# Optimization experiments

Measured on AMD Instinct MI355X. Metric: run time of the kernel, lower is better.

The kernel has to match this reference:

```python
import jax, jax.numpy as jnp
import numpy as np

DIM = 512
HEADS = 8
HEAD_DIM = DIM // HEADS
SCALE = DIM ** (-0.5)  # source uses full dim, not head_dim
LAMBDA_COND = 1.0


def setup_inputs() -> dict:
    key = jax.random.key(0)
    ks = jax.random.split(key, 16)
    b, n, m_a, m_s = 4, 2048, 2048, 256
    s = 0.02
    inp = {
        "x": jax.random.normal(ks[0], (b, n, DIM), jnp.float32),
        "audio_context": jax.random.normal(ks[1], (b, m_a, DIM), jnp.float32),
        "singer_context": jax.random.normal(ks[2], (b, m_s, DIM), jnp.float32),
        "Wq": jax.random.normal(ks[3], (DIM, DIM), jnp.float32) * s,
        "bq": jnp.zeros((DIM,), jnp.float32),
        "Wka": jax.random.normal(ks[4], (DIM, DIM), jnp.float32) * s,
        "bka": jnp.zeros((DIM,), jnp.float32),
        "Wva": jax.random.normal(ks[5], (DIM, DIM), jnp.float32) * s,
        "bva": jnp.zeros((DIM,), jnp.float32),
        "Wks": jax.random.normal(ks[6], (DIM, DIM), jnp.float32) * s,
        "bks": jnp.zeros((DIM,), jnp.float32),
        "Wvs": jax.random.normal(ks[7], (DIM, DIM), jnp.float32) * s,
        "bvs": jnp.zeros((DIM,), jnp.float32),
        "Wp": jax.random.normal(ks[8], (DIM, DIM), jnp.float32) * s,
        "bp": jnp.zeros((DIM,), jnp.float32),
    }
    return inp


def _heads(t):
    b, n, c = t.shape
    return t.reshape(b, n, HEADS, HEAD_DIM).transpose(0, 2, 1, 3)  # (b,h,n,d)


def _attend(q, ctx, Wk, bk, Wv, bv):
    k = _heads(ctx @ Wk.T + bk)
    v = _heads(ctx @ Wv.T + bv)
    attn = jax.nn.softmax(jnp.einsum("bhnd,bhmd->bhnm", q, k) * SCALE, axis=-1)
    o = jnp.einsum("bhnm,bhmd->bhnd", attn, v)
    b, h, n, d = o.shape
    return o.transpose(0, 2, 1, 3).reshape(b, n, h * d)


def reference(x, audio_context, singer_context, Wq, bq, Wka, bka, Wva, bva,
              Wks, bks, Wvs, bvs, Wp, bp):
    q = _heads(x @ Wq.T + bq)
    x_audio = _attend(q, audio_context, Wka, bka, Wva, bva)
    x_singer = _attend(q, singer_context, Wks, bks, Wvs, bvs)
    out = x_audio + LAMBDA_COND * x_singer
    return out @ Wp.T + bp
```

## Files before the change

kernel.cpp:

```cpp
#include <hip/hip_runtime.h>

#define DIM 512
#define NQ 2048
#define MA 2048
#define MS 256
#define QSCALE 0.06375864651f

typedef __attribute__((ext_vector_type(8))) short bf16x8;
typedef __attribute__((ext_vector_type(4))) float f32x4;
typedef __attribute__((ext_vector_type(16))) float f32x16;

__device__ __forceinline__ ushort f2b(float f) {
    uint u = __float_as_uint(f);
    u = (u + 0x7fffu + ((u >> 16) & 1u)) >> 16;
    return (ushort)u;
}

__device__ __forceinline__ uint pk2bf(float a, float b) {
#if __has_builtin(__builtin_amdgcn_cvt_pk_bf16_f32)
    typedef __attribute__((ext_vector_type(2))) __bf16 bf2;
    bf2 r = __builtin_amdgcn_cvt_pk_bf16_f32(a, b);
    uint u;
    __builtin_memcpy(&u, &r, 4);
    return u;
#else
    return ((__float_as_uint(a) + 0x8000u) >> 16) |
           ((__float_as_uint(b) + 0x8000u) & 0xffff0000u);
#endif
}

__device__ __forceinline__ float fexp2(float x) {
#if __has_builtin(__builtin_amdgcn_exp2f)
    return __builtin_amdgcn_exp2f(x);
#else
    return exp2f(x);
#endif
}

__device__ __forceinline__ void gload16(const ushort* g, ushort* l) {
    __builtin_amdgcn_global_load_lds(
        (const __attribute__((address_space(1))) void*)g,
        (__attribute__((address_space(3))) void*)l, 16, 0, 0);
}

__global__ __launch_bounds__(256) void cast_all(const float* __restrict__ w0,
                                                const float* __restrict__ w1,
                                                const float* __restrict__ w2,
                                                const float* __restrict__ w3,
                                                const float* __restrict__ w4,
                                                const float* __restrict__ w5,
                                                const float* __restrict__ x,
                                                const float* __restrict__ ac,
                                                const float* __restrict__ scx,
                                                ushort* __restrict__ dst) {
    int i = blockIdx.x * 256 + threadIdx.x;
    const float* s;
    int o;
    if (i < 393216) {
        int w = i >> 16;
        s = w < 3 ? (w == 0 ? w0 : (w == 1 ? w1 : w2))
                  : (w == 3 ? w3 : (w == 4 ? w4 : w5));
        o = i & 65535;
    } else if (i < 1441792) { s = x;   o = i - 393216; }
    else if (i < 2490368)   { s = ac;  o = i - 1441792; }
    else                    { s = scx; o = i - 2490368; }
    float4 v = ((const float4*)s)[o];
    ushort4 u;
    u.x = f2b(v.x); u.y = f2b(v.y); u.z = f2b(v.z); u.w = f2b(v.w);
    ((ushort4*)dst)[i] = u;
}

struct GD {
    const ushort* A; const ushort* B; const float* bias; void* out;
    long sB, sO;
    int N, bx, by, blk0, biasrow, scaleq, outf32, pad;
};

__global__ __launch_bounds__(256) void gemm_fused(GD d0, GD d1, GD d2, GD d3, GD d4) {
    __shared__ ushort At[128 * 32];
    __shared__ ushort Bt[128 * 32];
    GD d = d0;
    int bid = blockIdx.x;
    if (bid >= d1.blk0) d = d1;
    if (bid >= d2.blk0) d = d2;
    if (bid >= d3.blk0) d = d3;
    if (bid >= d4.blk0) d = d4;
    int local = bid - d.blk0;
    int x = local % d.bx;
    int rem = local / d.bx;
    int y = rem % d.by;
    int z = rem / d.by;

    int t = threadIdx.x;
    int wv = t >> 6, ln = t & 63, l = ln & 15, g = ln >> 4;
    int wrow = wv & 1, wcol = wv >> 1;
    int row0 = x * 128, col0 = y * 128;
    int srow = t >> 2;
    int slot = (t & 3) * 8;
    int sko = ((t ^ srow) & 3) * 8;
    int kc8 = ((g ^ (l & 3)) & 3) * 8;
    const ushort* Ab = d.A;
    const ushort* Bb = d.B + (size_t)z * d.sB;
    int N = d.N;

    f32x4 acc[4][4];
#pragma unroll
    for (int i = 0; i < 4; i++)
#pragma unroll
        for (int j = 0; j < 4; j++) acc[i][j] = (f32x4){0, 0, 0, 0};

    for (int k0 = 0; k0 < 512; k0 += 32) {
        __syncthreads();
#pragma unroll
        for (int c = 0; c < 2; c++) {
            gload16(Ab + (size_t)(row0 + srow + 64 * c) * 512 + k0 + sko,
                    At + (srow + 64 * c) * 32 + slot);
            gload16(Bb + (size_t)(col0 + srow + 64 * c) * 512 + k0 + sko,
                    Bt + (srow + 64 * c) * 32 + slot);
        }
        __syncthreads();
        bf16x8 ar[4], br[4];
#pragma unroll
        for (int i = 0; i < 4; i++)
            ar[i] = *(const bf16x8*)(At + (wrow * 64 + i * 16 + l) * 32 + kc8);
#pragma unroll
        for (int j = 0; j < 4; j++)
            br[j] = *(const bf16x8*)(Bt + (wcol * 64 + j * 16 + l) * 32 + kc8);
#pragma unroll
        for (int i = 0; i < 4; i++)
#pragma unroll
            for (int j = 0; j < 4; j++)
                acc[i][j] = __builtin_amdgcn_mfma_f32_16x16x32_bf16(ar[i], br[j], acc[i][j], 0, 0, 0);
    }
#pragma unroll
    for (int i = 0; i < 4; i++) {
#pragma unroll
        for (int j = 0; j < 4; j++) {
            int row = row0 + wrow * 64 + i * 16 + g * 4;
            int col = col0 + wcol * 64 + j * 16 + l;
#pragma unroll
            for (int r = 0; r < 4; r++) {
                float bv = d.biasrow ? d.bias[row + r] : d.bias[col];
                float o = acc[i][j][r] + bv;
                if (d.scaleq) o *= QSCALE;
                if (d.outf32)
                    ((float*)d.out + (size_t)z * d.sO)[(size_t)(row + r) * N + col] = o;
                else
                    ((ushort*)d.out + (size_t)z * d.sO)[(size_t)(row + r) * N + col] = f2b(o);
            }
        }
    }
}

__device__ __forceinline__ void attn_ctx32(const ushort* __restrict__ kg,
                                           const ushort* __restrict__ vg,
                                           int M, int nt, const bf16x8 (&aq)[4],
                                           ushort* __restrict__ Kl,
                                           ushort* __restrict__ Vl,
                                           f32x16 (&o)[2], float& li,
                                           int l5, int hi, int sr, int sc, int vbase) {
    bf16x8 k0 = *(const bf16x8*)kg;
    bf16x8 k1 = *(const bf16x8*)(kg + (size_t)32 * DIM);
    bf16x8 v0 = *(const bf16x8*)vg;
    bf16x8 v1 = *(const bf16x8*)(vg + (size_t)32 * M);
    __syncthreads();
    {
        *(bf16x8*)(Kl + sr * 72 + sc) = k0;
        *(bf16x8*)(Kl + (sr + 32) * 72 + sc) = k1;
        union { bf16x8 v; uint2 h[2]; } cv;
        cv.v = v0;
        *(uint2*)(Vl + sr * 72 + vbase) = cv.h[0];
        *(uint2*)(Vl + sr * 72 + vbase + 8) = cv.h[1];
        cv.v = v1;
        *(uint2*)(Vl + (sr + 32) * 72 + vbase) = cv.h[0];
        *(uint2*)(Vl + (sr + 32) * 72 + vbase + 8) = cv.h[1];
    }
    if (nt > 1) {
        k0 = *(const bf16x8*)(kg + (size_t)64 * DIM);
        k1 = *(const bf16x8*)(kg + (size_t)96 * DIM);
        v0 = *(const bf16x8*)(vg + 64);
        v1 = *(const bf16x8*)(vg + (size_t)32 * M + 64);
    }
    for (int i = 0; i < nt; i++) {
        __syncthreads();
        if (i + 1 < nt) {
            ushort* Kb = Kl + ((i + 1) & 1) * (64 * 72);
            ushort* Vb = Vl + ((i + 1) & 1) * (64 * 72);
            *(bf16x8*)(Kb + sr * 72 + sc) = k0;
            *(bf16x8*)(Kb + (sr + 32) * 72 + sc) = k1;
            union { bf16x8 v; uint2 h[2]; } cv;
            cv.v = v0;
            *(uint2*)(Vb + sr * 72 + vbase) = cv.h[0];
            *(uint2*)(Vb + sr * 72 + vbase + 8) = cv.h[1];
            cv.v = v1;
            *(uint2*)(Vb + (sr + 32) * 72 + vbase) = cv.h[0];
            *(uint2*)(Vb + (sr + 32) * 72 + vbase + 8) = cv.h[1];
        }
        if (i + 2 < nt) {
            size_t off = (size_t)(i + 2) * 64;
            k0 = *(const bf16x8*)(kg + off * DIM);
            k1 = *(const bf16x8*)(kg + (off + 32) * DIM);
            v0 = *(const bf16x8*)(vg + off);
            v1 = *(const bf16x8*)(vg + (size_t)32 * M + off);
        }
        const ushort* Kc = Kl + (i & 1) * (64 * 72);
        const ushort* Vc = Vl + (i & 1) * (64 * 72);
        uint2 pq[2][4];
#pragma unroll
        for (int c = 0; c < 2; c++) {
            bf16x8 kf[4];
#pragma unroll
            for (int kd = 0; kd < 4; kd++)
                kf[kd] = *(const bf16x8*)(Kc + (32 * c + l5) * 72 + kd * 16 + hi * 8);
            f32x16 s;
#pragma unroll
            for (int ii = 0; ii < 16; ii++) s[ii] = 0.f;
#pragma unroll
            for (int kd = 0; kd < 4; kd++)
                s = __builtin_amdgcn_mfma_f32_32x32x16_bf16(kf[kd], aq[kd], s, 0, 0, 0);
#pragma unroll
            for (int m = 0; m < 4; m++) {
                float p0 = fexp2(s[4 * m + 0]);
                float p1 = fexp2(s[4 * m + 1]);
                float p2 = fexp2(s[4 * m + 2]);
                float p3 = fexp2(s[4 * m + 3]);
                li += (p0 + p1) + (p2 + p3);
                pq[c][m].x = pk2bf(p0, p1);
                pq[c][m].y = pk2bf(p2, p3);
            }
        }
#pragma unroll
        for (int kc = 0; kc < 4; kc++) {
            int c = kc >> 1, m0 = 2 * (kc & 1);
            union { bf16x8 v; uint u[4]; } w;
            w.u[0] = pq[c][m0].x;     w.u[1] = pq[c][m0].y;
            w.u[2] = pq[c][m0 + 1].x; w.u[3] = pq[c][m0 + 1].y;
#pragma unroll
            for (int dn = 0; dn < 2; dn++) {
                bf16x8 vf = *(const bf16x8*)(Vc + (32 * dn + l5) * 72 + kc * 16 + hi * 8);
                o[dn] = __builtin_amdgcn_mfma_f32_32x32x16_bf16(w.v, vf, o[dn], 0, 0, 0);
            }
        }
    }
}

__global__ __launch_bounds__(512, 2) void attn_kernel(const ushort* __restrict__ q,
                                                      const ushort* __restrict__ Ka,
                                                      const ushort* __restrict__ VTa,
                                                      const ushort* __restrict__ Ks,
                                                      const ushort* __restrict__ VTs,
                                                      ushort* __restrict__ y) {
    __shared__ ushort smem[2 * 18432];
    int t = threadIdx.x;
    int grp = t >> 8;
    int tg = t & 255;
    int wg = tg >> 6;
    int ln = t & 63, l5 = ln & 31, hi = ln >> 5;
    ushort* Kl = smem + grp * 18432;
    ushort* Vl = Kl + 9216;
    float* osc = (float*)(smem + 18432);
    int h = blockIdx.y, bi = blockIdx.z;
    int q0 = blockIdx.x * 128 + wg * 32;
    bf16x8 aq[4];
    const ushort* qp = q + (size_t)(bi * NQ + q0 + l5) * DIM + h * 64 + hi * 8;
#pragma unroll
    for (int kd = 0; kd < 4; kd++) aq[kd] = *(const bf16x8*)(qp + kd * 16);
    int sr = tg >> 3, sc = (tg & 7) * 8;
    int vbase = (sc >> 4) * 16 + ((sc >> 3) & 1) * 4;

    f32x16 o[2];
#pragma unroll
    for (int dn = 0; dn < 2; dn++)
#pragma unroll
        for (int i = 0; i < 16; i++) o[dn][i] = 0.f;
    float li = 0.f;

    attn_ctx32(Ka + (size_t)bi * MA * DIM + (size_t)(grp * 1024 + sr) * DIM + h * 64 + sc,
               VTa + (size_t)bi * DIM * MA + (size_t)(h * 64 + sr) * MA + grp * 1024 + sc,
               MA, 16, aq, Kl, Vl, o, li, l5, hi, sr, sc, vbase);
    li += __shfl_xor(li, 32);
    __syncthreads();
    if (grp) {
        float* p = osc + (wg * 64 + ln) * 34;
#pragma unroll
        for (int dn = 0; dn < 2; dn++)
#pragma unroll
            for (int k = 0; k < 8; k++)
                *(float2*)(p + dn * 16 + 2 * k) = (float2){o[dn][2 * k], o[dn][2 * k + 1]};
        p[32] = li;
    }
    __syncthreads();
    float yv[2][16];
    if (!grp) {
        const float* p = osc + (wg * 64 + ln) * 34;
#pragma unroll
        for (int dn = 0; dn < 2; dn++)
#pragma unroll
            for (int k = 0; k < 16; k++) o[dn][k] += p[dn * 16 + k];
        li += p[32];
        float inv[16];
#pragma unroll
        for (int rg = 0; rg < 16; rg++)
            inv[rg] = 1.f / __shfl(li, (rg & 3) + 8 * (rg >> 2) + 4 * hi);
#pragma unroll
        for (int dn = 0; dn < 2; dn++)
#pragma unroll
            for (int rg = 0; rg < 16; rg++) yv[dn][rg] = o[dn][rg] * inv[rg];
    }

#pragma unroll
    for (int dn = 0; dn < 2; dn++)
#pragma unroll
        for (int i = 0; i < 16; i++) o[dn][i] = 0.f;
    li = 0.f;
    attn_ctx32(Ks + (size_t)bi * MS * DIM + (size_t)(grp * 128 + sr) * DIM + h * 64 + sc,
               VTs + (size_t)bi * DIM * MS + (size_t)(h * 64 + sr) * MS + grp * 128 + sc,
               MS, 2, aq, Kl, Vl, o, li, l5, hi, sr, sc, vbase);
    li += __shfl_xor(li, 32);
    __syncthreads();
    if (grp) {
        float* p = osc + (wg * 64 + ln) * 34;
#pragma unroll
        for (int dn = 0; dn < 2; dn++)
#pragma unroll
            for (int k = 0; k < 8; k++)
                *(float2*)(p + dn * 16 + 2 * k) = (float2){o[dn][2 * k], o[dn][2 * k + 1]};
        p[32] = li;
    }
    __syncthreads();
    if (!grp) {
        const float* p = osc + (wg * 64 + ln) * 34;
#pragma unroll
        for (int dn = 0; dn < 2; dn++)
#pragma unroll
            for (int k = 0; k < 16; k++) o[dn][k] += p[dn * 16 + k];
        li += p[32];
        float inv[16];
#pragma unroll
        for (int rg = 0; rg < 16; rg++)
            inv[rg] = 1.f / __shfl(li, (rg & 3) + 8 * (rg >> 2) + 4 * hi);
#pragma unroll
        for (int dn = 0; dn < 2; dn++)
#pragma unroll
            for (int rg = 0; rg < 16; rg++) {
                int qr = (rg & 3) + 8 * (rg >> 2) + 4 * hi;
                float ov = yv[dn][rg] + o[dn][rg] * inv[rg];
                y[(size_t)(bi * NQ + q0 + qr) * DIM + h * 64 + 32 * dn + l5] = f2b(ov);
            }
    }
}

extern "C" void kernel_launch(void* const* d_in, const int* in_sizes, int n_in,
                              void* d_out, int out_size, void* d_ws, size_t ws_size,
                              hipStream_t stream) {
    const float* x   = (const float*)d_in[0];
    const float* ac  = (const float*)d_in[1];
    const float* scx = (const float*)d_in[2];
    const float* Wq  = (const float*)d_in[3];
    const float* bq  = (const float*)d_in[4];
    const float* Wka = (const float*)d_in[5];
    const float* bka = (const float*)d_in[6];
    const float* Wva = (const float*)d_in[7];
    const float* bva = (const float*)d_in[8];
    const float* Wks = (const float*)d_in[9];
    const float* bks = (const float*)d_in[10];
    const float* Wvs = (const float*)d_in[11];
    const float* bvs = (const float*)d_in[12];
    const float* Wp  = (const float*)d_in[13];
    const float* bp  = (const float*)d_in[14];

    ushort* wb   = (ushort*)d_ws;
    ushort* wqb  = wb;
    ushort* wkab = wb + 262144;
    ushort* wvab = wb + 2 * 262144;
    ushort* wksb = wb + 3 * 262144;
    ushort* wvsb = wb + 4 * 262144;
    ushort* wpb  = wb + 5 * 262144;
    ushort* xb   = wb + 6 * 262144;
    ushort* acb  = xb + 4194304;
    ushort* scxb = acb + 4194304;
    ushort* qb   = scxb + 524288;
    ushort* kab  = qb + 4194304;
    ushort* vta  = kab + 4194304;
    ushort* ksb  = vta + 4194304;
    ushort* vts  = ksb + 524288;
    ushort* yb   = xb;

    cast_all<<<10240, 256, 0, stream>>>(Wq, Wka, Wva, Wks, Wvs, Wp, x, ac, scx, wb);

    GD gq   = {xb,   wqb,  bq,  qb,  0, 0,               512,  64, 4,  0,   0, 1, 0, 0};
    GD gka  = {acb,  wkab, bka, kab, 0, 0,               512,  64, 4,  256, 0, 0, 0, 0};
    GD gvta = {wvab, acb,  bva, vta, 2048L * 512, 512L * 2048, 2048, 4, 16, 512, 1, 0, 0, 0};
    GD gks  = {scxb, wksb, bks, ksb, 0, 0,               512,  8,  4,  768, 0, 0, 0, 0};
    GD gvts = {wvsb, scxb, bvs, vts, 256L * 512, 512L * 256,   256,  4,  2,  800, 1, 0, 0, 0};
    gemm_fused<<<832, 256, 0, stream>>>(gq, gka, gvta, gks, gvts);

    attn_kernel<<<dim3(16, 8, 4), 512, 0, stream>>>(qb, kab, vta, ksb, vts, yb);

    GD gpr = {yb, wpb, bp, d_out, 0, 0, 512, 64, 4, 0, 0, 0, 1, 0};
    GD gnv = {nullptr, nullptr, nullptr, nullptr, 0, 0, 0, 1, 1, 1 << 30, 0, 0, 0, 0};
    gemm_fused<<<256, 256, 0, stream>>>(gpr, gnv, gnv, gnv, gnv);
}
```

Before: 227.9 us.

## Process 64 queries per wave in attention, with async swizzled K/V loads

The attention kernel now has each wave handle 64 query rows (two 32-row halves) instead of 32. Each K/V fragment read from LDS is reused across both halves, and the grid shrinks to half as many blocks. K/V tiles are loaded straight into unpadded, XOR-swizzled LDS with asynchronous global-to-LDS loads. The V-transpose GEMM epilogue permutes its output columns to match the new LDS fragment layout. s_setprio hints are added around the MFMA bursts. The cost is more registers per wave (four output accumulators) and fewer blocks, which may reduce occupancy and parallelism.

```diff
diff --git a/kernel.cpp b/kernel.cpp
--- a/kernel.cpp
+++ b/kernel.cpp
@@ -73,7 +73,7 @@
 struct GD {
     const ushort* A; const ushort* B; const float* bias; void* out;
     long sB, sO;
-    int N, bx, by, blk0, biasrow, scaleq, outf32, pad;
+    int N, bx, by, blk0, biasrow, scaleq, outf32, permc;
 };
 
 __global__ __launch_bounds__(256) void gemm_fused(GD d0, GD d1, GD d2, GD d3, GD d4) {
@@ -99,6 +99,8 @@
     int slot = (t & 3) * 8;
     int sko = ((t ^ srow) & 3) * 8;
     int kc8 = ((g ^ (l & 3)) & 3) * 8;
+    int l4 = (l >> 2) & 3;
+    int lp = d.permc ? (l4 == 1 ? l + 4 : (l4 == 2 ? l - 4 : l)) : l;
     const ushort* Ab = d.A;
     const ushort* Bb = d.B + (size_t)z * d.sB;
     int N = d.N;
@@ -137,7 +139,7 @@
 #pragma unroll
         for (int j = 0; j < 4; j++) {
             int row = row0 + wrow * 64 + i * 16 + g * 4;
-            int col = col0 + wcol * 64 + j * 16 + l;
+            int col = col0 + wcol * 64 + j * 16 + lp;
 #pragma unroll
             for (int r = 0; r < 4; r++) {
                 float bv = d.biasrow ? d.bias[row + r] : d.bias[col];
@@ -152,201 +154,205 @@
     }
 }
 
-__device__ __forceinline__ void attn_ctx32(const ushort* __restrict__ kg,
-                                           const ushort* __restrict__ vg,
-                                           int M, int nt, const bf16x8 (&aq)[4],
-                                           ushort* __restrict__ Kl,
-                                           ushort* __restrict__ Vl,
-                                           f32x16 (&o)[2], float& li,
-                                           int l5, int hi, int sr, int sc, int vbase) {
-    bf16x8 k0 = *(const bf16x8*)kg;
-    bf16x8 k1 = *(const bf16x8*)(kg + (size_t)32 * DIM);
-    bf16x8 v0 = *(const bf16x8*)vg;
-    bf16x8 v1 = *(const bf16x8*)(vg + (size_t)32 * M);
-    __syncthreads();
-    {
-        *(bf16x8*)(Kl + sr * 72 + sc) = k0;
-        *(bf16x8*)(Kl + (sr + 32) * 72 + sc) = k1;
-        union { bf16x8 v; uint2 h[2]; } cv;
-        cv.v = v0;
-        *(uint2*)(Vl + sr * 72 + vbase) = cv.h[0];
-        *(uint2*)(Vl + sr * 72 + vbase + 8) = cv.h[1];
-        cv.v = v1;
-        *(uint2*)(Vl + (sr + 32) * 72 + vbase) = cv.h[0];
-        *(uint2*)(Vl + (sr + 32) * 72 + vbase + 8) = cv.h[1];
-    }
-    if (nt > 1) {
-        k0 = *(const bf16x8*)(kg + (size_t)64 * DIM);
-        k1 = *(const bf16x8*)(kg + (size_t)96 * DIM);
-        v0 = *(const bf16x8*)(vg + 64);
-        v1 = *(const bf16x8*)(vg + (size_t)32 * M + 64);
-    }
+__device__ __forceinline__ void attn_64q(const ushort* __restrict__ kgb,
+                                         const ushort* __restrict__ vgb,
+                                         int M, int nt, const bf16x8 (&aq)[2][4],
+                                         ushort* __restrict__ Kl,
+                                         ushort* __restrict__ Vl,
+                                         f32x16 (&o)[4], float (&li)[2],
+                                         int l5, int hi, int w, int ln) {
+    int r8 = ln >> 3;
+    int cc = 8 * ((ln & 7) ^ r8);
+    const ushort* ks0 = kgb + (size_t)(w * 16 + r8) * DIM + cc;
+    const ushort* vs0 = vgb + (size_t)(w * 16 + r8) * M + cc;
+    int rx = (l5 & 7) * 8;
+    int hb = hi * 8;
+    gload16(ks0, Kl + w * 1024);
+    gload16(ks0 + (size_t)8 * DIM, Kl + w * 1024 + 512);
+    gload16(vs0, Vl + w * 1024);
+    gload16(vs0 + (size_t)8 * M, Vl + w * 1024 + 512);
     for (int i = 0; i < nt; i++) {
         __syncthreads();
         if (i + 1 < nt) {
-            ushort* Kb = Kl + ((i + 1) & 1) * (64 * 72);
-            ushort* Vb = Vl + ((i + 1) & 1) * (64 * 72);
-            *(bf16x8*)(Kb + sr * 72 + sc) = k0;
-            *(bf16x8*)(Kb + (sr + 32) * 72 + sc) = k1;
-            union { bf16x8 v; uint2 h[2]; } cv;
-            cv.v = v0;
-            *(uint2*)(Vb + sr * 72 + vbase) = cv.h[0];
-            *(uint2*)(Vb + sr * 72 + vbase + 8) = cv.h[1];
-            cv.v = v1;
-            *(uint2*)(Vb + (sr + 32) * 72 + vbase) = cv.h[0];
-            *(uint2*)(Vb + (sr + 32) * 72 + vbase + 8) = cv.h[1];
-        }
-        if (i + 2 < nt) {
-            size_t off = (size_t)(i + 2) * 64;
-            k0 = *(const bf16x8*)(kg + off * DIM);
-            k1 = *(const bf16x8*)(kg + (off + 32) * DIM);
-            v0 = *(const bf16x8*)(vg + off);
-            v1 = *(const bf16x8*)(vg + (size_t)32 * M + off);
-        }
-        const ushort* Kc = Kl + (i & 1) * (64 * 72);
-        const ushort* Vc = Vl + (i & 1) * (64 * 72);
-        uint2 pq[2][4];
+            const ushort* ks = ks0 + (size_t)(i + 1) * 64 * DIM;
+            const ushort* vs = vs0 + (size_t)(i + 1) * 64;
+            ushort* Kb = Kl + ((i + 1) & 1) * 4096;
+            ushort* Vb = Vl + ((i + 1) & 1) * 4096;
+            gload16(ks, Kb + w * 1024);
+            gload16(ks + (size_t)8 * DIM, Kb + w * 1024 + 512);
+            gload16(vs, Vb + w * 1024);
+            gload16(vs + (size_t)8 * M, Vb + w * 1024 + 512);
+        }
+        const ushort* Kc = Kl + (i & 1) * 4096;
+        const ushort* Vc = Vl + (i & 1) * 4096;
+        uint2 pq[2][2][4];
 #pragma unroll
         for (int c = 0; c < 2; c++) {
             bf16x8 kf[4];
 #pragma unroll
             for (int kd = 0; kd < 4; kd++)
-                kf[kd] = *(const bf16x8*)(Kc + (32 * c + l5) * 72 + kd * 16 + hi * 8);
-            f32x16 s;
-#pragma unroll
-            for (int ii = 0; ii < 16; ii++) s[ii] = 0.f;
-#pragma unroll
-            for (int kd = 0; kd < 4; kd++)
-                s = __builtin_amdgcn_mfma_f32_32x32x16_bf16(kf[kd], aq[kd], s, 0, 0, 0);
-#pragma unroll
-            for (int m = 0; m < 4; m++) {
-                float p0 = fexp2(s[4 * m + 0]);
-                float p1 = fexp2(s[4 * m + 1]);
-                float p2 = fexp2(s[4 * m + 2]);
-                float p3 = fexp2(s[4 * m + 3]);
-                li += (p0 + p1) + (p2 + p3);
-                pq[c][m].x = pk2bf(p0, p1);
-                pq[c][m].y = pk2bf(p2, p3);
+                kf[kd] = *(const bf16x8*)(Kc + (32 * c + l5) * 64 + ((kd * 16 + hb) ^ rx));
+#pragma unroll
+            for (int qh = 0; qh < 2; qh++) {
+                f32x16 s;
+#pragma unroll
+                for (int ii = 0; ii < 16; ii++) s[ii] = 0.f;
+                __builtin_amdgcn_s_setprio(1);
+#pragma unroll
+                for (int kd = 0; kd < 4; kd++)
+                    s = __builtin_amdgcn_mfma_f32_32x32x16_bf16(kf[kd], aq[qh][kd], s, 0, 0, 0);
+                __builtin_amdgcn_s_setprio(0);
+#pragma unroll
+                for (int m = 0; m < 4; m++) {
+                    float p0 = fexp2(s[4 * m + 0]);
+                    float p1 = fexp2(s[4 * m + 1]);
+                    float p2 = fexp2(s[4 * m + 2]);
+                    float p3 = fexp2(s[4 * m + 3]);
+                    li[qh] += (p0 + p1) + (p2 + p3);
+                    pq[qh][c][m].x = pk2bf(p0, p1);
+                    pq[qh][c][m].y = pk2bf(p2, p3);
+                }
             }
         }
 #pragma unroll
         for (int kc = 0; kc < 4; kc++) {
             int c = kc >> 1, m0 = 2 * (kc & 1);
-            union { bf16x8 v; uint u[4]; } w;
-            w.u[0] = pq[c][m0].x;     w.u[1] = pq[c][m0].y;
-            w.u[2] = pq[c][m0 + 1].x; w.u[3] = pq[c][m0 + 1].y;
-#pragma unroll
-            for (int dn = 0; dn < 2; dn++) {
-                bf16x8 vf = *(const bf16x8*)(Vc + (32 * dn + l5) * 72 + kc * 16 + hi * 8);
-                o[dn] = __builtin_amdgcn_mfma_f32_32x32x16_bf16(w.v, vf, o[dn], 0, 0, 0);
+            bf16x8 vf0 = *(const bf16x8*)(Vc + l5 * 64 + ((kc * 16 + hb) ^ rx));
+            bf16x8 vf1 = *(const bf16x8*)(Vc + (32 + l5) * 64 + ((kc * 16 + hb) ^ rx));
+            __builtin_amdgcn_s_setprio(1);
+#pragma unroll
+            for (int qh = 0; qh < 2; qh++) {
+                union { bf16x8 v; uint u[4]; } wv;
+                wv.u[0] = pq[qh][c][m0].x;     wv.u[1] = pq[qh][c][m0].y;
+                wv.u[2] = pq[qh][c][m0 + 1].x; wv.u[3] = pq[qh][c][m0 + 1].y;
+                o[qh * 2 + 0] = __builtin_amdgcn_mfma_f32_32x32x16_bf16(wv.v, vf0, o[qh * 2 + 0], 0, 0, 0);
+                o[qh * 2 + 1] = __builtin_amdgcn_mfma_f32_32x32x16_bf16(wv.v, vf1, o[qh * 2 + 1], 0, 0, 0);
             }
-        }
-    }
-}
-
-__global__ __launch_bounds__(512, 2) void attn_kernel(const ushort* __restrict__ q,
-                                                      const ushort* __restrict__ Ka,
-                                                      const ushort* __restrict__ VTa,
-                                                      const ushort* __restrict__ Ks,
-                                                      const ushort* __restrict__ VTs,
-                                                      ushort* __restrict__ y) {
-    __shared__ ushort smem[2 * 18432];
+            __builtin_amdgcn_s_setprio(0);
+        }
+    }
+}
+
+__global__ __launch_bounds__(512) void attn_kernel(const ushort* __restrict__ q,
+                                                   const ushort* __restrict__ Ka,
+                                                   const ushort* __restrict__ VTa,
+                                                   const ushort* __restrict__ Ks,
+                                                   const ushort* __restrict__ VTs,
+                                                   ushort* __restrict__ y) {
+    __shared__ ushort smem[67584];
     int t = threadIdx.x;
     int grp = t >> 8;
     int tg = t & 255;
-    int wg = tg >> 6;
+    int w = (t >> 6) & 3;
     int ln = t & 63, l5 = ln & 31, hi = ln >> 5;
-    ushort* Kl = smem + grp * 18432;
-    ushort* Vl = Kl + 9216;
-    float* osc = (float*)(smem + 18432);
+    ushort* Kl = smem + grp * 16384;
+    ushort* Vl = Kl + 8192;
+    float* Bx = (float*)(smem + 32768);
+    float* Ax = (float*)smem;
     int h = blockIdx.y, bi = blockIdx.z;
-    int q0 = blockIdx.x * 128 + wg * 32;
-    bf16x8 aq[4];
-    const ushort* qp = q + (size_t)(bi * NQ + q0 + l5) * DIM + h * 64 + hi * 8;
-#pragma unroll
-    for (int kd = 0; kd < 4; kd++) aq[kd] = *(const bf16x8*)(qp + kd * 16);
-    int sr = tg >> 3, sc = (tg & 7) * 8;
-    int vbase = (sc >> 4) * 16 + ((sc >> 3) & 1) * 4;
-
-    f32x16 o[2];
-#pragma unroll
-    for (int dn = 0; dn < 2; dn++)
-#pragma unroll
-        for (int i = 0; i < 16; i++) o[dn][i] = 0.f;
-    float li = 0.f;
-
-    attn_ctx32(Ka + (size_t)bi * MA * DIM + (size_t)(grp * 1024 + sr) * DIM + h * 64 + sc,
-               VTa + (size_t)bi * DIM * MA + (size_t)(h * 64 + sr) * MA + grp * 1024 + sc,
-               MA, 16, aq, Kl, Vl, o, li, l5, hi, sr, sc, vbase);
-    li += __shfl_xor(li, 32);
+    int q0w = blockIdx.x * 256 + w * 64;
+
+    bf16x8 aq[2][4];
+#pragma unroll
+    for (int qh = 0; qh < 2; qh++) {
+        const ushort* qp = q + (size_t)(bi * NQ + q0w + qh * 32 + l5) * DIM + h * 64 + hi * 8;
+#pragma unroll
+        for (int kd = 0; kd < 4; kd++) aq[qh][kd] = *(const bf16x8*)(qp + kd * 16);
+    }
+
+    f32x16 o[4];
+#pragma unroll
+    for (int k = 0; k < 4; k++)
+#pragma unroll
+        for (int i = 0; i < 16; i++) o[k][i] = 0.f;
+    float li[2] = {0.f, 0.f};
+
+    attn_64q(Ka + (size_t)bi * MA * DIM + (size_t)(grp * 1024) * DIM + h * 64,
+             VTa + (size_t)bi * DIM * MA + (size_t)(h * 64) * MA + grp * 1024,
+             MA, 16, aq, Kl, Vl, o, li, l5, hi, w, ln);
+    li[0] += __shfl_xor(li[0], 32);
+    li[1] += __shfl_xor(li[1], 32);
     __syncthreads();
+    float* slot = Bx + tg * 68;
     if (grp) {
-        float* p = osc + (wg * 64 + ln) * 34;
-#pragma unroll
-        for (int dn = 0; dn < 2; dn++)
-#pragma unroll
-            for (int k = 0; k < 8; k++)
-                *(float2*)(p + dn * 16 + 2 * k) = (float2){o[dn][2 * k], o[dn][2 * k + 1]};
-        p[32] = li;
-    }
-    __syncthreads();
-    float yv[2][16];
-    if (!grp) {
-        const float* p = osc + (wg * 64 + ln) * 34;
-#pragma unroll
-        for (int dn = 0; dn < 2; dn++)
-#pragma unroll
-            for (int k = 0; k < 16; k++) o[dn][k] += p[dn * 16 + k];
-        li += p[32];
-        float inv[16];
-#pragma unroll
-        for (int rg = 0; rg < 16; rg++)
-            inv[rg] = 1.f / __shfl(li, (rg & 3) + 8 * (rg >> 2) + 4 * hi);
-#pragma unroll
-        for (int dn = 0; dn < 2; dn++)
-#pragma unroll
-            for (int rg = 0; rg < 16; rg++) yv[dn][rg] = o[dn][rg] * inv[rg];
-    }
-
-#pragma unroll
-    for (int dn = 0; dn < 2; dn++)
-#pragma unroll
-        for (int i = 0; i < 16; i++) o[dn][i] = 0.f;
-    li = 0.f;
-    attn_ctx32(Ks + (size_t)bi * MS * DIM + (size_t)(grp * 128 + sr) * DIM + h * 64 + sc,
-               VTs + (size_t)bi * DIM * MS + (size_t)(h * 64 + sr) * MS + grp * 128 + sc,
-               MS, 2, aq, Kl, Vl, o, li, l5, hi, sr, sc, vbase);
-    li += __shfl_xor(li, 32);
-    __syncthreads();
-    if (grp) {
-        float* p = osc + (wg * 64 + ln) * 34;
-#pragma unroll
-        for (int dn = 0; dn < 2; dn++)
-#pragma unroll
-            for (int k = 0; k < 8; k++)
-                *(float2*)(p + dn * 16 + 2 * k) = (float2){o[dn][2 * k], o[dn][2 * k + 1]};
-        p[32] = li;
+#pragma unroll
+        for (int k = 0; k < 4; k++)
+#pragma unroll
+            for (int r = 0; r < 8; r++)
+                *(float2*)(slot + k * 16 + 2 * r) = (float2){o[k][2 * r], o[k][2 * r + 1]};
+        slot[64] = li[0];
+        slot[65] = li[1];
     }
     __syncthreads();
     if (!grp) {
-        const float* p = osc + (wg * 64 + ln) * 34;
-#pragma unroll
-        for (int dn = 0; dn < 2; dn++)
-#pragma unroll
-            for (int k = 0; k < 16; k++) o[dn][k] += p[dn * 16 + k];
-        li += p[32];
-        float inv[16];
-#pragma unroll
-        for (int rg = 0; rg < 16; rg++)
-            inv[rg] = 1.f / __shfl(li, (rg & 3) + 8 * (rg >> 2) + 4 * hi);
-#pragma unroll
-        for (int dn = 0; dn < 2; dn++)
-#pragma unroll
-            for (int rg = 0; rg < 16; rg++) {
-                int qr = (rg & 3) + 8 * (rg >> 2) + 4 * hi;
-                float ov = yv[dn][rg] + o[dn][rg] * inv[rg];
-                y[(size_t)(bi * NQ + q0 + qr) * DIM + h * 64 + 32 * dn + l5] = f2b(ov);
-            }
+#pragma unroll
+        for (int k = 0; k < 4; k++)
+#pragma unroll
+            for (int r = 0; r < 16; r++) o[k][r] += slot[k * 16 + r];
+        li[0] += slot[64];
+        li[1] += slot[65];
+#pragma unroll
+        for (int qh = 0; qh < 2; qh++) {
+            float inv[16];
+#pragma unroll
+            for (int rg = 0; rg < 16; rg++)
+                inv[rg] = 1.f / __shfl(li[qh], (rg & 3) + 8 * (rg >> 2) + 4 * hi);
+#pragma unroll
+            for (int dn = 0; dn < 2; dn++)
+#pragma unroll
+                for (int rg = 0; rg < 16; rg++) o[qh * 2 + dn][rg] *= inv[rg];
+        }
+#pragma unroll
+        for (int k = 0; k < 4; k++)
+#pragma unroll
+            for (int r = 0; r < 8; r++)
+                *(float2*)(slot + k * 16 + 2 * r) = (float2){o[k][2 * r], o[k][2 * r + 1]};
+    }
+
+#pragma unroll
+    for (int k = 0; k < 4; k++)
+#pragma unroll
+        for (int i = 0; i < 16; i++) o[k][i] = 0.f;
+    li[0] = li[1] = 0.f;
+    attn_64q(Ks + (size_t)bi * MS * DIM + (size_t)(grp * 128) * DIM + h * 64,
+             VTs + (size_t)bi * DIM * MS + (size_t)(h * 64) * MS + grp * 128,
+             MS, 2, aq, Kl, Vl, o, li, l5, hi, w, ln);
+    li[0] += __shfl_xor(li[0], 32);
+    li[1] += __shfl_xor(li[1], 32);
+    __syncthreads();
+    float* As = Ax + tg * 64;
+    if (grp) {
+#pragma unroll
+        for (int k = 0; k < 4; k++)
+#pragma unroll
+            for (int r = 0; r < 8; r++)
+                *(float2*)(As + k * 16 + 2 * r) = (float2){o[k][2 * r], o[k][2 * r + 1]};
+        slot[66] = li[0];
+        slot[67] = li[1];
+    }
+    __syncthreads();
+    if (!grp) {
+#pragma unroll
+        for (int k = 0; k < 4; k++)
+#pragma unroll
+            for (int r = 0; r < 16; r++) o[k][r] += As[k * 16 + r];
+        li[0] += slot[66];
+        li[1] += slot[67];
+#pragma unroll
+        for (int qh = 0; qh < 2; qh++) {
+            float inv[16];
+#pragma unroll
+            for (int rg = 0; rg < 16; rg++)
+                inv[rg] = 1.f / __shfl(li[qh], (rg & 3) + 8 * (rg >> 2) + 4 * hi);
+#pragma unroll
+            for (int dn = 0; dn < 2; dn++)
+#pragma unroll
+                for (int rg = 0; rg < 16; rg++) {
+                    int qr = (rg & 3) + 8 * (rg >> 2) + 4 * hi;
+                    float ov = slot[(qh * 2 + dn) * 16 + rg] + o[qh * 2 + dn][rg] * inv[rg];
+                    y[(size_t)(bi * NQ + q0w + qh * 32 + qr) * DIM + h * 64 + 32 * dn + l5] = f2b(ov);
+                }
+        }
     }
 }
 
@@ -390,12 +396,12 @@
 
     GD gq   = {xb,   wqb,  bq,  qb,  0, 0,               512,  64, 4,  0,   0, 1, 0, 0};
     GD gka  = {acb,  wkab, bka, kab, 0, 0,               512,  64, 4,  256, 0, 0, 0, 0};
-    GD gvta = {wvab, acb,  bva, vta, 2048L * 512, 512L * 2048, 2048, 4, 16, 512, 1, 0, 0, 0};
+    GD gvta = {wvab, acb,  bva, vta, 2048L * 512, 512L * 2048, 2048, 4, 16, 512, 1, 0, 0, 1};
     GD gks  = {scxb, wksb, bks, ksb, 0, 0,               512,  8,  4,  768, 0, 0, 0, 0};
-    GD gvts = {wvsb, scxb, bvs, vts, 256L * 512, 512L * 256,   256,  4,  2,  800, 1, 0, 0, 0};
+    GD gvts = {wvsb, scxb, bvs, vts, 256L * 512, 512L * 256,   256,  4,  2,  800, 1, 0, 0, 1};
     gemm_fused<<<832, 256, 0, stream>>>(gq, gka, gvta, gks, gvts);
 
-    attn_kernel<<<dim3(16, 8, 4), 512, 0, stream>>>(qb, kab, vta, ksb, vts, yb);
+    attn_kernel<<<dim3(8, 8, 4), 512, 0, stream>>>(qb, kab, vta, ksb, vts, yb);
 
     GD gpr = {yb, wpb, bp, d_out, 0, 0, 512, 64, 4, 0, 0, 0, 1, 0};
     GD gnv = {nullptr, nullptr, nullptr, nullptr, 0, 0, 0, 1, 1, 1 << 30, 0, 0, 0, 0};
```

Result: no change. 226.7 us (-0.5%).

## Fuse fp32-to-bf16 casts into GEMM loads with register-prefetched staging

Applied to the files above, without the earlier changes.

Removes the separate cast kernel and has the GEMM read fp32 inputs and weights directly, converting to bf16 in registers before writing to LDS. The direct global-to-LDS loads are replaced with register loads, prefetched one k-step ahead to overlap global latency with the MFMAs. This saves a full read-write pass over the activations and one launch. In exchange each GEMM reads twice the bytes and spends VALU on conversion, with extra register pressure. A permc column-permutation field is added but is zero in every launch.

```diff
diff --git a/kernel.cpp b/kernel.cpp
--- a/kernel.cpp
+++ b/kernel.cpp
@@ -37,46 +37,14 @@
 #endif
 }
 
-__device__ __forceinline__ void gload16(const ushort* g, ushort* l) {
-    __builtin_amdgcn_global_load_lds(
-        (const __attribute__((address_space(1))) void*)g,
-        (__attribute__((address_space(3))) void*)l, 16, 0, 0);
-}
-
-__global__ __launch_bounds__(256) void cast_all(const float* __restrict__ w0,
-                                                const float* __restrict__ w1,
-                                                const float* __restrict__ w2,
-                                                const float* __restrict__ w3,
-                                                const float* __restrict__ w4,
-                                                const float* __restrict__ w5,
-                                                const float* __restrict__ x,
-                                                const float* __restrict__ ac,
-                                                const float* __restrict__ scx,
-                                                ushort* __restrict__ dst) {
-    int i = blockIdx.x * 256 + threadIdx.x;
-    const float* s;
-    int o;
-    if (i < 393216) {
-        int w = i >> 16;
-        s = w < 3 ? (w == 0 ? w0 : (w == 1 ? w1 : w2))
-                  : (w == 3 ? w3 : (w == 4 ? w4 : w5));
-        o = i & 65535;
-    } else if (i < 1441792) { s = x;   o = i - 393216; }
-    else if (i < 2490368)   { s = ac;  o = i - 1441792; }
-    else                    { s = scx; o = i - 2490368; }
-    float4 v = ((const float4*)s)[o];
-    ushort4 u;
-    u.x = f2b(v.x); u.y = f2b(v.y); u.z = f2b(v.z); u.w = f2b(v.w);
-    ((ushort4*)dst)[i] = u;
-}
-
 struct GD {
-    const ushort* A; const ushort* B; const float* bias; void* out;
+    const void* A; const void* B; const float* bias; void* out;
     long sB, sO;
-    int N, bx, by, blk0, biasrow, scaleq, outf32, pad;
+    int N, bx, by, blk0, biasrow, scaleq, outf32, permc;
 };
 
-__global__ __launch_bounds__(256) void gemm_fused(GD d0, GD d1, GD d2, GD d3, GD d4) {
+template <int AF32, int BF32>
+__global__ __launch_bounds__(256) void gemm_t(GD d0, GD d1, GD d2, GD d3, GD d4) {
     __shared__ ushort At[128 * 32];
     __shared__ ushort Bt[128 * 32];
     GD d = d0;
@@ -99,9 +67,68 @@
     int slot = (t & 3) * 8;
     int sko = ((t ^ srow) & 3) * 8;
     int kc8 = ((g ^ (l & 3)) & 3) * 8;
-    const ushort* Ab = d.A;
-    const ushort* Bb = d.B + (size_t)z * d.sB;
+    int l4 = (l >> 2) & 3;
+    int lp = d.permc ? (l4 == 1 ? l + 4 : (l4 == 2 ? l - 4 : l)) : l;
     int N = d.N;
+    int so0 = srow * 32 + slot;
+    int so1 = (srow + 64) * 32 + slot;
+
+    float4 fa[4], fb[4];
+    bf16x8 ha[2], hb[2];
+
+    auto issue = [&](int k0) {
+        if (AF32) {
+            const float* A0 = (const float*)d.A + (size_t)(row0 + srow) * 512 + k0 + sko;
+            const float* A1 = (const float*)d.A + (size_t)(row0 + srow + 64) * 512 + k0 + sko;
+            fa[0] = *(const float4*)A0; fa[1] = *(const float4*)(A0 + 4);
+            fa[2] = *(const float4*)A1; fa[3] = *(const float4*)(A1 + 4);
+        } else {
+            const ushort* A0 = (const ushort*)d.A + (size_t)(row0 + srow) * 512 + k0 + sko;
+            const ushort* A1 = (const ushort*)d.A + (size_t)(row0 + srow + 64) * 512 + k0 + sko;
+            ha[0] = *(const bf16x8*)A0;
+            ha[1] = *(const bf16x8*)A1;
+        }
+        if (BF32) {
+            const float* Bb = (const float*)d.B + (size_t)z * d.sB;
+            const float* B0 = Bb + (size_t)(col0 + srow) * 512 + k0 + sko;
+            const float* B1 = Bb + (size_t)(col0 + srow + 64) * 512 + k0 + sko;
+            fb[0] = *(const float4*)B0; fb[1] = *(const float4*)(B0 + 4);
+            fb[2] = *(const float4*)B1; fb[3] = *(const float4*)(B1 + 4);
+        } else {
+            const ushort* Bb = (const ushort*)d.B + (size_t)z * d.sB;
+            const ushort* B0 = Bb + (size_t)(col0 + srow) * 512 + k0 + sko;
+            const ushort* B1 = Bb + (size_t)(col0 + srow + 64) * 512 + k0 + sko;
+            hb[0] = *(const bf16x8*)B0;
+            hb[1] = *(const bf16x8*)B1;
+        }
+    };
+
+    auto wstage = [&]() {
+        if (AF32) {
+            union { bf16x8 v; uint u[4]; } w0, w1;
+            w0.u[0] = pk2bf(fa[0].x, fa[0].y); w0.u[1] = pk2bf(fa[0].z, fa[0].w);
+            w0.u[2] = pk2bf(fa[1].x, fa[1].y); w0.u[3] = pk2bf(fa[1].z, fa[1].w);
+            w1.u[0] = pk2bf(fa[2].x, fa[2].y); w1.u[1] = pk2bf(fa[2].z, fa[2].w);
+            w1.u[2] = pk2bf(fa[3].x, fa[3].y); w1.u[3] = pk2bf(fa[3].z, fa[3].w);
+            *(bf16x8*)(At + so0) = w0.v;
+            *(bf16x8*)(At + so1) = w1.v;
+        } else {
+            *(bf16x8*)(At + so0) = ha[0];
+            *(bf16x8*)(At + so1) = ha[1];
+        }
+        if (BF32) {
+            union { bf16x8 v; uint u[4]; } w0, w1;
+            w0.u[0] = pk2bf(fb[0].x, fb[0].y); w0.u[1] = pk2bf(fb[0].z, fb[0].w);
+            w0.u[2] = pk2bf(fb[1].x, fb[1].y); w0.u[3] = pk2bf(fb[1].z, fb[1].w);
+            w1.u[0] = pk2bf(fb[2].x, fb[2].y); w1.u[1] = pk2bf(fb[2].z, fb[2].w);
+            w1.u[2] = pk2bf(fb[3].x, fb[3].y); w1.u[3] = pk2bf(fb[3].z, fb[3].w);
+            *(bf16x8*)(Bt + so0) = w0.v;
+            *(bf16x8*)(Bt + so1) = w1.v;
+        } else {
+            *(bf16x8*)(Bt + so0) = hb[0];
+            *(bf16x8*)(Bt + so1) = hb[1];
+        }
+    };
 
     f32x4 acc[4][4];
 #pragma unroll
@@ -109,16 +136,14 @@
 #pragma unroll
         for (int j = 0; j < 4; j++) acc[i][j] = (f32x4){0, 0, 0, 0};
 
+    issue(0);
+
+#pragma unroll 1
     for (int k0 = 0; k0 < 512; k0 += 32) {
         __syncthreads();
-#pragma unroll
-        for (int c = 0; c < 2; c++) {
-            gload16(Ab + (size_t)(row0 + srow + 64 * c) * 512 + k0 + sko,
-                    At + (srow + 64 * c) * 32 + slot);
-            gload16(Bb + (size_t)(col0 + srow + 64 * c) * 512 + k0 + sko,
-                    Bt + (srow + 64 * c) * 32 + slot);
-        }
+        wstage();
         __syncthreads();
+        if (k0 + 32 < 512) issue(k0 + 32);
         bf16x8 ar[4], br[4];
 #pragma unroll
         for (int i = 0; i < 4; i++)
@@ -137,7 +162,7 @@
 #pragma unroll
         for (int j = 0; j < 4; j++) {
             int row = row0 + wrow * 64 + i * 16 + g * 4;
-            int col = col0 + wcol * 64 + j * 16 + l;
+            int col = col0 + wcol * 64 + j * 16 + lp;
 #pragma unroll
             for (int r = 0; r < 4; r++) {
                 float bv = d.biasrow ? d.bias[row + r] : d.bias[col];
@@ -369,35 +394,23 @@
     const float* Wp  = (const float*)d_in[13];
     const float* bp  = (const float*)d_in[14];
 
-    ushort* wb   = (ushort*)d_ws;
-    ushort* wqb  = wb;
-    ushort* wkab = wb + 262144;
-    ushort* wvab = wb + 2 * 262144;
-    ushort* wksb = wb + 3 * 262144;
-    ushort* wvsb = wb + 4 * 262144;
-    ushort* wpb  = wb + 5 * 262144;
-    ushort* xb   = wb + 6 * 262144;
-    ushort* acb  = xb + 4194304;
-    ushort* scxb = acb + 4194304;
-    ushort* qb   = scxb + 524288;
-    ushort* kab  = qb + 4194304;
-    ushort* vta  = kab + 4194304;
-    ushort* ksb  = vta + 4194304;
-    ushort* vts  = ksb + 524288;
-    ushort* yb   = xb;
-
-    cast_all<<<10240, 256, 0, stream>>>(Wq, Wka, Wva, Wks, Wvs, Wp, x, ac, scx, wb);
-
-    GD gq   = {xb,   wqb,  bq,  qb,  0, 0,               512,  64, 4,  0,   0, 1, 0, 0};
-    GD gka  = {acb,  wkab, bka, kab, 0, 0,               512,  64, 4,  256, 0, 0, 0, 0};
-    GD gvta = {wvab, acb,  bva, vta, 2048L * 512, 512L * 2048, 2048, 4, 16, 512, 1, 0, 0, 0};
-    GD gks  = {scxb, wksb, bks, ksb, 0, 0,               512,  8,  4,  768, 0, 0, 0, 0};
-    GD gvts = {wvsb, scxb, bvs, vts, 256L * 512, 512L * 256,   256,  4,  2,  800, 1, 0, 0, 0};
-    gemm_fused<<<832, 256, 0, stream>>>(gq, gka, gvta, gks, gvts);
+    ushort* qb  = (ushort*)d_ws;
+    ushort* kab = qb + 4194304;
+    ushort* vta = kab + 4194304;
+    ushort* ksb = vta + 4194304;
+    ushort* vts = ksb + 524288;
+    ushort* yb  = vts + 524288;
+
+    GD gq   = {x,   Wq,  bq,  qb,  0, 0,                    512,  64, 4,  0,   0, 1, 0, 0};
+    GD gka  = {ac,  Wka, bka, kab, 0, 0,                    512,  64, 4,  256, 0, 0, 0, 0};
+    GD gvta = {Wva, ac,  bva, vta, 2048L * 512, 512L * 2048, 2048, 4, 16, 512, 1, 0, 0, 0};
+    GD gks  = {scx, Wks, bks, ksb, 0, 0,                    512,  8,  4,  768, 0, 0, 0, 0};
+    GD gvts = {Wvs, scx, bvs, vts, 256L * 512, 512L * 256,   256,  4,  2,  800, 1, 0, 0, 0};
+    gemm_t<1, 1><<<832, 256, 0, stream>>>(gq, gka, gvta, gks, gvts);
 
     attn_kernel<<<dim3(16, 8, 4), 512, 0, stream>>>(qb, kab, vta, ksb, vts, yb);
 
-    GD gpr = {yb, wpb, bp, d_out, 0, 0, 512, 64, 4, 0, 0, 0, 1, 0};
+    GD gpr = {yb, Wp, bp, d_out, 0, 0, 512, 64, 4, 0, 0, 0, 1, 0};
     GD gnv = {nullptr, nullptr, nullptr, nullptr, 0, 0, 0, 1, 1, 1 << 30, 0, 0, 0, 0};
-    gemm_fused<<<256, 256, 0, stream>>>(gpr, gnv, gnv, gnv, gnv);
-}
+    gemm_t<0, 1><<<256, 256, 0, stream>>>(gpr, gnv, gnv, gnv, gnv);
+}
```

Result: no change. 229.6 us (+0.7%).
